# Performance work log

Measured on AMD Instinct MI355X. Metric: run time of the kernel, lower is better.

Reference implementation:

```python
import jax, jax.numpy as jnp
import numpy as np

B, IN_DIM, H, OUT_DIM, T = 2048, 1024, 2048, 1024, 10


def setup_inputs() -> dict:
    key = jax.random.key(0)
    ks = jax.random.split(key, 16)
    s = lambda d: 1.0 / np.sqrt(d)
    inp = {
        "x": jax.random.normal(ks[0], (B, IN_DIM), jnp.float32),
        "z0": jax.random.normal(ks[1], (B, H), jnp.float32),
        "noise": jax.random.normal(ks[2], (T, B, H), jnp.float32),
        # input_embed: Linear(IN,H) -> SiLU -> Linear(H,H)
        "w1_in": jax.random.normal(ks[3], (IN_DIM, H), jnp.float32) * s(IN_DIM),
        "b1_in": jnp.zeros((H,), jnp.float32),
        "w2_in": jax.random.normal(ks[4], (H, H), jnp.float32) * s(H),
        "b2_in": jnp.zeros((H,), jnp.float32),
        # T blocks: Linear(2H,H) -> SiLU -> Linear(H,H), stacked over T
        "wA": jax.random.normal(ks[5], (T, 2 * H, H), jnp.float32) * s(2 * H),
        "bA": jnp.zeros((T, H), jnp.float32),
        "wB": jax.random.normal(ks[6], (T, H, H), jnp.float32) * s(H),
        "bB": jnp.zeros((T, H), jnp.float32),
        # classifier Linear(H, OUT)
        "wC": jax.random.normal(ks[7], (H, OUT_DIM), jnp.float32) * s(H),
        "bC": jnp.zeros((OUT_DIM,), jnp.float32),
    }
    return inp


def _forward(x, z0, noise, w1_in, b1_in, w2_in, b2_in, wA, bA, wB, bB, wC, bC):
    # input embedding
    h = jax.nn.silu(x @ w1_in + b1_in)
    x_embed = h @ w2_in + b2_in  # (B, H)

    alpha = jnp.linspace(0.99, 0.9, T).astype(x.dtype)          # (T,)
    noise_scale = jnp.sqrt(1.0 - alpha)                          # (T,)

    def step(z, per_t):
        wA_t, bA_t, wB_t, bB_t, n_t, a_t, ns_t = per_t
        u = jax.nn.silu(jnp.concatenate([z, x_embed], axis=-1) @ wA_t + bA_t)
        u = u @ wB_t + bB_t
        z_next = a_t * u + (1.0 - a_t) * z + ns_t * n_t
        return z_next, None

    z_final, _ = jax.lax.scan(step, z0, (wA, bA, wB, bB, noise, alpha, noise_scale))
    return z_final @ wC + bC  # (B, OUT_DIM)


def reference(x, z0, noise, w1_in, b1_in, w2_in, b2_in, wA, bA, wB, bB, wC, bC):
    return _forward(x, z0, noise, w1_in, b1_in, w2_in, b2_in, wA, bA, wB, bB, wC, bC)
```

## Files before the change

### kernel.cpp

```cpp
#include <hip/hip_runtime.h>
#include <math.h>

typedef _Float16 f16;
typedef _Float16 f16x4 __attribute__((ext_vector_type(4)));
typedef _Float16 f16x8 __attribute__((ext_vector_type(8)));
typedef float f32x4 __attribute__((ext_vector_type(4)));
typedef float fvec4 __attribute__((ext_vector_type(4)));

#define EP_SILU 0
#define EP_LIN  1
#define EP_ZUP  2
#define EP_OUT  3
#define EP_ADDP 4

struct TDesc {
  const float* W;
  f16* WT;
  long long sW, sWT;
  int R, C, nMat;
};

__device__ __forceinline__ void gll16(const void* g, void* l) {
  __builtin_amdgcn_global_load_lds((__attribute__((address_space(1))) void*)g,
                                   (__attribute__((address_space(3))) void*)l,
                                   16, 0, 0);
}

__device__ __forceinline__ void stage_tile(const f16* __restrict__ g, int ld,
                                           f16* ldsTile, int tid, int wid) {
#pragma unroll
  for (int p = 0; p < 2; ++p) {
    int row = p * 64 + (tid >> 2);
    int col = (tid & 3) * 8;
    gll16(g + (size_t)row * ld + col, ldsTile + p * 2048 + wid * 512);
  }
}

__device__ __forceinline__ void stage8(const f16* __restrict__ g, int ld,
                                       f16* ldsTile, int tid) {
  int row = tid >> 2, col = (tid & 3) * 8;
  gll16(g + (size_t)row * ld + col, ldsTile + tid * 8);
}

__device__ __forceinline__ void tpose_tile(const float* __restrict__ W,
                                           f16* __restrict__ WT, int R, int C,
                                           int r0, int c0, f16 (*t)[72],
                                           int tid) {
#pragma unroll
  for (int p = 0; p < 2; ++p) {
    int lin = p * 2048 + tid * 4;
    int r = lin >> 6, c4 = lin & 63;
    fvec4 v = *(const fvec4*)(W + (size_t)(r0 + r) * C + c0 + c4);
    t[c4 + 0][r] = (f16)v[0];
    t[c4 + 1][r] = (f16)v[1];
    t[c4 + 2][r] = (f16)v[2];
    t[c4 + 3][r] = (f16)v[3];
  }
  __syncthreads();
#pragma unroll
  for (int p = 0; p < 2; ++p) {
    int lin = p * 2048 + tid * 4;
    int c = lin >> 6, r4 = lin & 63;
    f16x4 h;
    h[0] = t[c][r4 + 0];
    h[1] = t[c][r4 + 1];
    h[2] = t[c][r4 + 2];
    h[3] = t[c][r4 + 3];
    *(f16x4*)(WT + (size_t)(c0 + c) * R + r0 + r4) = h;
  }
  __syncthreads();
}

__device__ void run_role(const TDesc d, int rid, int nr, f16 (*t)[72],
                         int tid) {
  if (d.nMat <= 0 || d.W == nullptr) return;
  int tR = d.R >> 6, tC = d.C >> 6;
  int tpm = tR * tC, tot = tpm * d.nMat;
  for (int i = rid; i < tot; i += nr) {
    int m = i / tpm, rem = i - m * tpm;
    int r0 = (rem % tR) << 6, c0 = (rem / tR) << 6;
    tpose_tile(d.W + (size_t)m * d.sW, d.WT + (size_t)m * d.sWT, d.R, d.C, r0,
               c0, t, tid);
  }
}

#define GEMM8_ITER(KP, VM, DO_STAGE)                                          \
  {                                                                           \
    asm volatile("s_waitcnt vmcnt(" #VM ")" ::: "memory");                    \
    __builtin_amdgcn_s_barrier();                                             \
    const int slot_ = (KP) & 1;                                               \
    const f16* LA_ = base + slot_ * 16384 + h * 4096;                         \
    const f16* LB_ = base + slot_ * 16384 + 8192 + h * 4096;                  \
    f16x8 a_[4], b_[4];                                                       \
    _Pragma("unroll") for (int m_ = 0; m_ < 4; ++m_) a_[m_] =                 \
        *(const f16x8*)(LA_ + ((wr * 64 + m_ * 16 + lr) * 32 + kg * 8));      \
    _Pragma("unroll") for (int n_ = 0; n_ < 4; ++n_) b_[n_] =                 \
        *(const f16x8*)(LB_ + ((wc * 64 + n_ * 16 + lr) * 32 + kg * 8));      \
    asm volatile("s_waitcnt lgkmcnt(0)" ::: "memory");                        \
    __builtin_amdgcn_s_barrier();                                             \
    if (DO_STAGE) stageAB((KP) + 2, slot_);                                   \
    _Pragma("unroll") for (int m_ = 0; m_ < 4; ++m_)                          \
        _Pragma("unroll") for (int n_ = 0; n_ < 4; ++n_) acc[m_][n_] =        \
            __builtin_amdgcn_mfma_f32_16x16x32_f16(a_[m_], b_[n_],            \
                                                   acc[m_][n_], 0, 0, 0);     \
  }

template <int EP>
__global__ void __launch_bounds__(512)
gemm8(const f16* __restrict__ A, int lda, const f16* __restrict__ BT, int ldb,
      long long sBT, int K, int N, int gx, int nbGemm,
      const float* __restrict__ bias, long long sBias,
      const f16* __restrict__ addP, f16* __restrict__ outH,
      float* __restrict__ outF, long long sOut, const f16* __restrict__ zOld,
      const float* __restrict__ noise, float aT, float nsT, TDesc dA,
      TDesc dB) {
  __shared__ __align__(16) char smem[65536];
  const int tid = threadIdx.x;
  const int bid = blockIdx.x;

  if (bid >= nbGemm) {
    if (blockIdx.z == 0) {
      int rid = bid - nbGemm, nr = (int)gridDim.x - nbGemm;
      f16(*t)[72] = reinterpret_cast<f16(*)[72]>(smem);
      run_role(dA, rid, nr, t, tid);
      run_role(dB, rid, nr, t, tid);
    }
    return;
  }

  const int z = blockIdx.z;
  const f16* BTz = BT + (size_t)z * sBT;
  f16* outHz = outH ? outH + (size_t)z * sOut : nullptr;
  float* outFz = outF ? outF + (size_t)z * sOut : nullptr;

  const int cpx = nbGemm >> 3;
  const int swz = (bid & 7) * cpx + (bid >> 3);
  const int by = swz / gx, bx = swz % gx;
  const int m0 = by * 128, n0 = bx * 128;

  const int lane = tid & 63, wid = tid >> 6;
  const int q = wid & 3, h = wid >> 2;
  const int wr = q >> 1, wc = q & 1;
  const int lr = lane & 15, kg = lane >> 4;

  f16* base = (f16*)smem;
  f32x4 acc[4][4] = {};

  const int nkp = K >> 6;
  auto stageAB = [&](int kp, int slot) {
    int k0 = kp << 6;
    f16* s = base + slot * 16384;
    stage8(A + (size_t)m0 * lda + k0, lda, s, tid);
    stage8(A + (size_t)m0 * lda + k0 + 32, lda, s + 4096, tid);
    stage8(BTz + (size_t)n0 * ldb + k0, ldb, s + 8192, tid);
    stage8(BTz + (size_t)n0 * ldb + k0 + 32, ldb, s + 12288, tid);
  };

  stageAB(0, 0);
  stageAB(1, 1);
  int kp = 0;
  for (; kp < nkp - 1; ++kp) GEMM8_ITER(kp, 4, (kp + 2 < nkp));
  GEMM8_ITER(kp, 0, 0);

  float* red = (float*)smem;
  if (h == 1) {
#pragma unroll
    for (int m = 0; m < 4; ++m)
#pragma unroll
      for (int n = 0; n < 4; ++n) {
        int row = wr * 64 + m * 16 + kg * 4;
        int col = wc * 64 + n * 16 + lr;
        int rs = row ^ ((col & 7) << 2);
        *(f32x4*)&red[(size_t)col * 128 + rs] = acc[m][n];
      }
  }
  __syncthreads();
  if (h != 0) return;

  float bcol[4];
  if constexpr (EP != EP_ADDP) {
    const float* biasz = bias + (size_t)z * sBias;
#pragma unroll
    for (int n = 0; n < 4; ++n) bcol[n] = biasz[n0 + wc * 64 + n * 16 + lr];
  }

#pragma unroll
  for (int m = 0; m < 4; ++m) {
    int rowb = m0 + wr * 64 + m * 16 + kg * 4;
    int rowl = wr * 64 + m * 16 + kg * 4;
#pragma unroll
    for (int n = 0; n < 4; ++n) {
      int col = n0 + wc * 64 + n * 16 + lr;
      int coll = wc * 64 + n * 16 + lr;
      int rsl = rowl ^ ((coll & 7) << 2);
      f32x4 osum = acc[m][n] + *(const f32x4*)&red[(size_t)coll * 128 + rsl];
#pragma unroll
      for (int r = 0; r < 4; ++r) {
        size_t idx = (size_t)(rowb + r) * N + col;
        float v = osum[r];
        if constexpr (EP == EP_ADDP) v += (float)addP[idx];
        else v += bcol[n];
        if constexpr (EP == EP_SILU || EP == EP_ADDP) {
          v = v / (1.0f + __expf(-v));
          outHz[idx] = (f16)v;
        } else if constexpr (EP == EP_LIN) {
          outHz[idx] = (f16)v;
        } else if constexpr (EP == EP_OUT) {
          outFz[idx] = v;
        } else {
          float zn = aT * v + (1.0f - aT) * (float)zOld[idx] + nsT * noise[idx];
          outHz[idx] = (f16)zn;
        }
      }
    }
  }
}

template <int EP>
__global__ void __launch_bounds__(256)
gemm_bt(const f16* __restrict__ A0, const f16* __restrict__ A1, int Ksplit,
        int lda, const f16* __restrict__ BT, int ldb, long long sBT, int K,
        int N, int gx, const float* __restrict__ bias, long long sBias,
        f16* __restrict__ outH, float* __restrict__ outF, long long sOut,
        const float* __restrict__ zOld, const float* __restrict__ noise,
        float aT, float nsT) {
  __shared__ __align__(16) f16 lds[2][2][128 * 32];
  const int tid = threadIdx.x;
  const int z = blockIdx.z;
  const f16* BTz = BT + (size_t)z * sBT;
  f16* outHz = outH ? outH + (size_t)z * sOut : nullptr;
  float* outFz = outF ? outF + (size_t)z * sOut : nullptr;

  const int lane = tid & 63, wid = tid >> 6;
  const int wr = wid >> 1, wc = wid & 1;
  const int lr = lane & 15, kg = lane >> 4;
  const int by = blockIdx.x / gx, bx = blockIdx.x - by * gx;
  const int m0 = by * 128, n0 = bx * 128;

  f32x4 acc[4][4] = {};
  const int nk = K >> 5;
  auto stageAB = [&](int kt, int buf) {
    int k0 = kt << 5;
    const f16* Abase = (k0 < Ksplit)
                           ? (A0 + (size_t)m0 * lda + k0)
                           : (A1 + (size_t)m0 * lda + (k0 - Ksplit));
    stage_tile(Abase, lda, &lds[buf][0][0], tid, wid);
    stage_tile(BTz + (size_t)n0 * ldb + k0, ldb, &lds[buf][1][0], tid, wid);
  };

  stageAB(0, 0);
  __syncthreads();
  int cur = 0;
  for (int kt = 0; kt < nk; ++kt) {
    if (kt + 1 < nk) stageAB(kt + 1, cur ^ 1);
    const f16* LA = &lds[cur][0][0];
    const f16* LB = &lds[cur][1][0];
    f16x8 a[4], b[4];
#pragma unroll
    for (int m = 0; m < 4; ++m)
      a[m] = *(const f16x8*)(LA + ((wr * 64 + m * 16 + lr) * 32 + kg * 8));
#pragma unroll
    for (int n = 0; n < 4; ++n)
      b[n] = *(const f16x8*)(LB + ((wc * 64 + n * 16 + lr) * 32 + kg * 8));
#pragma unroll
    for (int m = 0; m < 4; ++m)
#pragma unroll
      for (int n = 0; n < 4; ++n)
        acc[m][n] = __builtin_amdgcn_mfma_f32_16x16x32_f16(a[m], b[n],
                                                           acc[m][n], 0, 0, 0);
    __syncthreads();
    cur ^= 1;
  }

  float bcol[4];
  const float* biasz = bias + (size_t)z * sBias;
#pragma unroll
  for (int n = 0; n < 4; ++n) bcol[n] = biasz[n0 + wc * 64 + n * 16 + lr];

#pragma unroll
  for (int m = 0; m < 4; ++m) {
    int rowb = m0 + wr * 64 + m * 16 + kg * 4;
#pragma unroll
    for (int n = 0; n < 4; ++n) {
      int col = n0 + wc * 64 + n * 16 + lr;
#pragma unroll
      for (int r = 0; r < 4; ++r) {
        size_t idx = (size_t)(rowb + r) * N + col;
        float v = acc[m][n][r] + bcol[n];
        if constexpr (EP == EP_SILU) {
          v = v / (1.0f + __expf(-v));
          outHz[idx] = (f16)v;
        } else if constexpr (EP == EP_LIN) {
          outHz[idx] = (f16)v;
        } else if constexpr (EP == EP_OUT) {
          outFz[idx] = v;
        } else {
          float zn = aT * v + (1.0f - aT) * zOld[idx] + nsT * noise[idx];
          outFz[idx] = zn;
          outHz[idx] = (f16)zn;
        }
      }
    }
  }
}

__global__ void __launch_bounds__(512) tconv_role(TDesc d) {
  __shared__ __align__(16) f16 t[64][72];
  run_role(d, blockIdx.x, gridDim.x, t, threadIdx.x);
}

__global__ void __launch_bounds__(256)
cvt4(const float* __restrict__ in, f16* __restrict__ outp, int n4) {
  int i = blockIdx.x * 256 + threadIdx.x;
  if (i >= n4) return;
  fvec4 v = *(const fvec4*)(in + (size_t)i * 4);
  f16x4 h;
  h[0] = (f16)v[0];
  h[1] = (f16)v[1];
  h[2] = (f16)v[2];
  h[3] = (f16)v[3];
  *(f16x4*)(outp + (size_t)i * 4) = h;
}

__global__ void __launch_bounds__(256)
zinit4(const float* __restrict__ z0, float* __restrict__ z32,
       f16* __restrict__ z16, int n4) {
  int i = blockIdx.x * 256 + threadIdx.x;
  if (i >= n4) return;
  fvec4 v = *(const fvec4*)(z0 + (size_t)i * 4);
  *(fvec4*)(z32 + (size_t)i * 4) = v;
  f16x4 h;
  h[0] = (f16)v[0];
  h[1] = (f16)v[1];
  h[2] = (f16)v[2];
  h[3] = (f16)v[3];
  *(f16x4*)(z16 + (size_t)i * 4) = h;
}

extern "C" void kernel_launch(void* const* d_in, const int* in_sizes, int n_in,
                              void* d_out, int out_size, void* d_ws,
                              size_t ws_size, hipStream_t stream) {
  const int B = 2048, IN = 1024, H = 2048, OUT = 1024, T = 10;
  const float* x = (const float*)d_in[0];
  const float* z0 = (const float*)d_in[1];
  const float* noise = (const float*)d_in[2];
  const float* w1 = (const float*)d_in[3];
  const float* b1 = (const float*)d_in[4];
  const float* w2 = (const float*)d_in[5];
  const float* b2 = (const float*)d_in[6];
  const float* wA = (const float*)d_in[7];
  const float* bA = (const float*)d_in[8];
  const float* wB = (const float*)d_in[9];
  const float* bB = (const float*)d_in[10];
  const float* wC = (const float*)d_in[11];
  const float* bC = (const float*)d_in[12];
  float* out = (float*)d_out;

  char* ws = (char*)d_ws;
  size_t off = 0;
  auto alloc = [&](size_t bytes) {
    void* p = ws + off;
    off += (bytes + 255) & ~(size_t)255;
    return p;
  };
  TDesc none = {nullptr, nullptr, 0, 0, 0, 0, 0};

  const size_t FAST_NEED = 273000000ull;
  if (ws_size >= FAST_NEED) {
    f16* x16 = (f16*)alloc((size_t)B * IN * 2);
    f16* h16 = (f16*)alloc((size_t)B * H * 2);
    f16* xe16 = (f16*)alloc((size_t)B * H * 2);
    f16* z16 = (f16*)alloc((size_t)B * H * 2);
    f16* u16 = (f16*)alloc((size_t)B * H * 2);
    f16* p16 = (f16*)alloc((size_t)T * B * H * 2);
    f16* w1T = (f16*)alloc((size_t)IN * H * 2);
    f16* w2T = (f16*)alloc((size_t)H * H * 2);
    f16* wCT = (f16*)alloc((size_t)H * OUT * 2);
    f16* wAbotT = (f16*)alloc((size_t)T * H * H * 2);
    f16* wAtopT[2] = {(f16*)alloc((size_t)H * H * 2),
                      (f16*)alloc((size_t)H * H * 2)};
    f16* wBT2[2] = {(f16*)alloc((size_t)H * H * 2),
                    (f16*)alloc((size_t)H * H * 2)};

    cvt4<<<B * IN / 4 / 256, 256, 0, stream>>>(x, x16, B * IN / 4);
    cvt4<<<B * H / 4 / 256, 256, 0, stream>>>(z0, z16, B * H / 4);
    tconv_role<<<512, 512, 0, stream>>>(TDesc{w1, w1T, 0, 0, IN, H, 1});

    gemm8<EP_SILU><<<512, 512, 0, stream>>>(
        x16, IN, w1T, IN, 0, IN, H, 16, 256, b1, 0, nullptr, h16, nullptr, 0,
        nullptr, nullptr, 0.f, 0.f, TDesc{w2, w2T, 0, 0, H, H, 1},
        TDesc{wA + (size_t)H * H, wAbotT, (long long)2 * H * H,
              (long long)H * H, H, H, 4});
    gemm8<EP_LIN><<<512, 512, 0, stream>>>(
        h16, H, w2T, H, 0, H, H, 16, 256, b2, 0, nullptr, xe16, nullptr, 0,
        nullptr, nullptr, 0.f, 0.f, TDesc{wC, wCT, 0, 0, H, OUT, 1},
        TDesc{wA + (size_t)H * H + (size_t)4 * 2 * H * H,
              wAbotT + (size_t)4 * H * H, (long long)2 * H * H,
              (long long)H * H, H, H, 6});
    tconv_role<<<512, 512, 0, stream>>>(TDesc{wA, wAtopT[0], 0, 0, H, H, 1});

    gemm8<EP_LIN><<<dim3(256, 1, T), 512, 0, stream>>>(
        xe16, H, wAbotT, H, (long long)H * H, H, H, 16, 256, bA, H, nullptr,
        p16, nullptr, (long long)B * H, nullptr, nullptr, 0.f, 0.f, none,
        none);

    for (int t = 0; t < T; ++t) {
      float alpha = (float)(0.99 - 0.01 * (double)t);
      float ns = sqrtf(1.0f - alpha);
      gemm8<EP_ADDP><<<320, 512, 0, stream>>>(
          z16, H, wAtopT[t & 1], H, 0, H, H, 16, 256, nullptr, 0,
          p16 + (size_t)t * B * H, u16, nullptr, 0, nullptr, nullptr, 0.f,
          0.f, TDesc{wB + (size_t)t * H * H, wBT2[t & 1], 0, 0, H, H, 1},
          none);
      TDesc nextA = (t < T - 1)
                        ? TDesc{wA + (size_t)(t + 1) * 2 * H * H,
                                wAtopT[(t + 1) & 1], 0, 0, H, H, 1}
                        : none;
      gemm8<EP_ZUP><<<320, 512, 0, stream>>>(
          u16, H, wBT2[t & 1], H, 0, H, H, 16, 256, bB + (size_t)t * H, 0,
          nullptr, z16, nullptr, 0, z16, noise + (size_t)t * B * H, alpha, ns,
          nextA, none);
    }
    gemm8<EP_OUT><<<128, 512, 0, stream>>>(
        z16, H, wCT, H, 0, H, OUT, 8, 128, bC, 0, nullptr, nullptr, out, 0,
        nullptr, nullptr, 0.f, 0.f, none, none);
  } else {
    f16* x16 = (f16*)alloc((size_t)B * IN * 2);
    f16* h16 = (f16*)alloc((size_t)B * H * 2);
    f16* xe16 = (f16*)alloc((size_t)B * H * 2);
    f16* z16 = (f16*)alloc((size_t)B * H * 2);
    f16* u16 = (f16*)alloc((size_t)B * H * 2);
    float* z32 = (float*)alloc((size_t)B * H * 4);
    f16* w1T = (f16*)alloc((size_t)IN * H * 2);
    f16* w2T = (f16*)alloc((size_t)H * H * 2);
    f16* wCT = (f16*)alloc((size_t)H * OUT * 2);
    f16* wAT = (f16*)alloc((size_t)2 * H * H * 2);
    f16* wBT = (f16*)alloc((size_t)H * H * 2);

    cvt4<<<B * IN / 4 / 256, 256, 0, stream>>>(x, x16, B * IN / 4);
    zinit4<<<B * H / 4 / 256, 256, 0, stream>>>(z0, z32, z16, B * H / 4);
    tconv_role<<<512, 512, 0, stream>>>(TDesc{w1, w1T, 0, 0, IN, H, 1});
    tconv_role<<<1024, 512, 0, stream>>>(TDesc{w2, w2T, 0, 0, H, H, 1});
    tconv_role<<<512, 512, 0, stream>>>(TDesc{wC, wCT, 0, 0, H, OUT, 1});

    gemm_bt<EP_SILU><<<dim3(256, 1, 1), 256, 0, stream>>>(
        x16, x16, IN, IN, w1T, IN, 0, IN, H, 16, b1, 0, h16, nullptr, 0,
        nullptr, nullptr, 0.f, 0.f);
    gemm_bt<EP_LIN><<<dim3(256, 1, 1), 256, 0, stream>>>(
        h16, h16, H, H, w2T, H, 0, H, H, 16, b2, 0, xe16, nullptr, 0, nullptr,
        nullptr, 0.f, 0.f);

    for (int t = 0; t < T; ++t) {
      float alpha = (float)(0.99 - 0.01 * (double)t);
      float ns = sqrtf(1.0f - alpha);
      tconv_role<<<1024, 512, 0, stream>>>(
          TDesc{wA + (size_t)t * 2 * H * H, wAT, 0, 0, 2 * H, H, 1});
      gemm_bt<EP_SILU><<<dim3(256, 1, 1), 256, 0, stream>>>(
          z16, xe16, H, H, wAT, 2 * H, 0, 2 * H, H, 16, bA + (size_t)t * H, 0,
          u16, nullptr, 0, nullptr, nullptr, 0.f, 0.f);
      tconv_role<<<1024, 512, 0, stream>>>(
          TDesc{wB + (size_t)t * H * H, wBT, 0, 0, H, H, 1});
      gemm_bt<EP_ZUP><<<dim3(256, 1, 1), 256, 0, stream>>>(
          u16, u16, H, H, wBT, H, 0, H, H, 16, bB + (size_t)t * H, 0, z16,
          z32, 0, z32, noise + (size_t)t * B * H, alpha, ns);
    }
    gemm_bt<EP_OUT><<<dim3(128, 1, 1), 256, 0, stream>>>(
        z16, z16, H, H, wCT, H, 0, H, OUT, 8, bC, 0, nullptr, out, 0, nullptr,
        nullptr, 0.f, 0.f);
  }
}
```

Before: 1.148 ms.

## Replace split-K 512-thread GEMM with 64x128-tile 256-thread GEMM and swizzled LDS

Replaces the 8-wave, 128x128-tile GEMM, which split K across two wave halves and reduced them through LDS, with a 4-wave kernel using 64x128 tiles, K-step 32, double buffering and XOR-swizzled LDS addressing. Grid sizes double so more blocks cover the 256 CUs, the cross-wave reduction is gone, and the transpose helper kernels move to 256 threads. In exchange, each block reuses fewer A rows per staged B tile, the loop synchronises once per shorter K step, and the explicit vmcnt-based prefetch pipelining is dropped.

```diff
diff --git a/kernel.cpp b/kernel.cpp
--- a/kernel.cpp
+++ b/kernel.cpp
@@ -36,19 +36,13 @@
   }
 }
 
-__device__ __forceinline__ void stage8(const f16* __restrict__ g, int ld,
-                                       f16* ldsTile, int tid) {
-  int row = tid >> 2, col = (tid & 3) * 8;
-  gll16(g + (size_t)row * ld + col, ldsTile + tid * 8);
-}
-
 __device__ __forceinline__ void tpose_tile(const float* __restrict__ W,
                                            f16* __restrict__ WT, int R, int C,
                                            int r0, int c0, f16 (*t)[72],
                                            int tid) {
 #pragma unroll
-  for (int p = 0; p < 2; ++p) {
-    int lin = p * 2048 + tid * 4;
+  for (int p = 0; p < 4; ++p) {
+    int lin = p * 1024 + tid * 4;
     int r = lin >> 6, c4 = lin & 63;
     fvec4 v = *(const fvec4*)(W + (size_t)(r0 + r) * C + c0 + c4);
     t[c4 + 0][r] = (f16)v[0];
@@ -58,8 +52,8 @@
   }
   __syncthreads();
 #pragma unroll
-  for (int p = 0; p < 2; ++p) {
-    int lin = p * 2048 + tid * 4;
+  for (int p = 0; p < 4; ++p) {
+    int lin = p * 1024 + tid * 4;
     int c = lin >> 6, r4 = lin & 63;
     f16x4 h;
     h[0] = t[c][r4 + 0];
@@ -84,37 +78,16 @@
   }
 }
 
-#define GEMM8_ITER(KP, VM, DO_STAGE)                                          \
-  {                                                                           \
-    asm volatile("s_waitcnt vmcnt(" #VM ")" ::: "memory");                    \
-    __builtin_amdgcn_s_barrier();                                             \
-    const int slot_ = (KP) & 1;                                               \
-    const f16* LA_ = base + slot_ * 16384 + h * 4096;                         \
-    const f16* LB_ = base + slot_ * 16384 + 8192 + h * 4096;                  \
-    f16x8 a_[4], b_[4];                                                       \
-    _Pragma("unroll") for (int m_ = 0; m_ < 4; ++m_) a_[m_] =                 \
-        *(const f16x8*)(LA_ + ((wr * 64 + m_ * 16 + lr) * 32 + kg * 8));      \
-    _Pragma("unroll") for (int n_ = 0; n_ < 4; ++n_) b_[n_] =                 \
-        *(const f16x8*)(LB_ + ((wc * 64 + n_ * 16 + lr) * 32 + kg * 8));      \
-    asm volatile("s_waitcnt lgkmcnt(0)" ::: "memory");                        \
-    __builtin_amdgcn_s_barrier();                                             \
-    if (DO_STAGE) stageAB((KP) + 2, slot_);                                   \
-    _Pragma("unroll") for (int m_ = 0; m_ < 4; ++m_)                          \
-        _Pragma("unroll") for (int n_ = 0; n_ < 4; ++n_) acc[m_][n_] =        \
-            __builtin_amdgcn_mfma_f32_16x16x32_f16(a_[m_], b_[n_],            \
-                                                   acc[m_][n_], 0, 0, 0);     \
-  }
-
 template <int EP>
-__global__ void __launch_bounds__(512)
-gemm8(const f16* __restrict__ A, int lda, const f16* __restrict__ BT, int ldb,
+__global__ void __launch_bounds__(256)
+gemm4(const f16* __restrict__ A, int lda, const f16* __restrict__ BT, int ldb,
       long long sBT, int K, int N, int gx, int nbGemm,
       const float* __restrict__ bias, long long sBias,
       const f16* __restrict__ addP, f16* __restrict__ outH,
       float* __restrict__ outF, long long sOut, const f16* __restrict__ zOld,
       const float* __restrict__ noise, float aT, float nsT, TDesc dA,
       TDesc dB) {
-  __shared__ __align__(16) char smem[65536];
+  __shared__ __align__(16) char smem[24576];
   const int tid = threadIdx.x;
   const int bid = blockIdx.x;
 
@@ -136,46 +109,62 @@
   const int cpx = nbGemm >> 3;
   const int swz = (bid & 7) * cpx + (bid >> 3);
   const int by = swz / gx, bx = swz % gx;
-  const int m0 = by * 128, n0 = bx * 128;
+  const int m0 = by * 64, n0 = bx * 128;
 
   const int lane = tid & 63, wid = tid >> 6;
-  const int q = wid & 3, h = wid >> 2;
-  const int wr = q >> 1, wc = q & 1;
+  const int wr = wid >> 1, wc = wid & 1;
   const int lr = lane & 15, kg = lane >> 4;
-
-  f16* base = (f16*)smem;
-  f32x4 acc[4][4] = {};
-
-  const int nkp = K >> 6;
-  auto stageAB = [&](int kp, int slot) {
-    int k0 = kp << 6;
-    f16* s = base + slot * 16384;
-    stage8(A + (size_t)m0 * lda + k0, lda, s, tid);
-    stage8(A + (size_t)m0 * lda + k0 + 32, lda, s + 4096, tid);
-    stage8(BTz + (size_t)n0 * ldb + k0, ldb, s + 8192, tid);
-    stage8(BTz + (size_t)n0 * ldb + k0 + 32, ldb, s + 12288, tid);
+  const int xq = (lr >> 1) & 3;
+
+  f16* lds = (f16*)smem;
+  f32x4 acc[2][4] = {};
+
+  const int nk = K >> 5;
+  auto stageAB = [&](int kt, int buf) {
+    int k0 = kt << 5;
+    f16* sA = lds + buf * 6144;
+    f16* sB = sA + 2048;
+    {
+      int row = tid >> 2;
+      int q = (tid & 3) ^ ((tid >> 3) & 3);
+      gll16(A + (size_t)(m0 + row) * lda + k0 + q * 8, sA + tid * 8);
+    }
+#pragma unroll
+    for (int p = 0; p < 2; ++p) {
+      int pos = p * 256 + tid;
+      int row = pos >> 2;
+      int q = (pos & 3) ^ ((pos >> 3) & 3);
+      gll16(BTz + (size_t)(n0 + row) * ldb + k0 + q * 8, sB + pos * 8);
+    }
   };
 
   stageAB(0, 0);
-  stageAB(1, 1);
-  int kp = 0;
-  for (; kp < nkp - 1; ++kp) GEMM8_ITER(kp, 4, (kp + 2 < nkp));
-  GEMM8_ITER(kp, 0, 0);
-
-  float* red = (float*)smem;
-  if (h == 1) {
-#pragma unroll
-    for (int m = 0; m < 4; ++m)
-#pragma unroll
-      for (int n = 0; n < 4; ++n) {
-        int row = wr * 64 + m * 16 + kg * 4;
-        int col = wc * 64 + n * 16 + lr;
-        int rs = row ^ ((col & 7) << 2);
-        *(f32x4*)&red[(size_t)col * 128 + rs] = acc[m][n];
-      }
-  }
   __syncthreads();
-  if (h != 0) return;
+  int cur = 0;
+  for (int kt = 0; kt < nk; ++kt) {
+    if (kt + 1 < nk) stageAB(kt + 1, cur ^ 1);
+    const f16* LA = lds + cur * 6144;
+    const f16* LB = LA + 2048;
+    f16x8 a[2], b[4];
+#pragma unroll
+    for (int m = 0; m < 2; ++m) {
+      int row = wr * 32 + m * 16 + lr;
+      a[m] = *(const f16x8*)(LA + row * 32 + (kg ^ xq) * 8);
+    }
+#pragma unroll
+    for (int n = 0; n < 4; ++n) {
+      int row = wc * 64 + n * 16 + lr;
+      b[n] = *(const f16x8*)(LB + row * 32 + (kg ^ xq) * 8);
+    }
+#pragma unroll
+    for (int m = 0; m < 2; ++m)
+#pragma unroll
+      for (int n = 0; n < 4; ++n)
+        acc[m][n] = __builtin_amdgcn_mfma_f32_16x16x32_f16(a[m], b[n],
+                                                           acc[m][n], 0, 0, 0);
+    __syncthreads();
+    cur ^= 1;
+  }
 
   float bcol[4];
   if constexpr (EP != EP_ADDP) {
@@ -185,19 +174,15 @@
   }
 
 #pragma unroll
-  for (int m = 0; m < 4; ++m) {
-    int rowb = m0 + wr * 64 + m * 16 + kg * 4;
-    int rowl = wr * 64 + m * 16 + kg * 4;
+  for (int m = 0; m < 2; ++m) {
+    int rowb = m0 + wr * 32 + m * 16 + kg * 4;
 #pragma unroll
     for (int n = 0; n < 4; ++n) {
       int col = n0 + wc * 64 + n * 16 + lr;
-      int coll = wc * 64 + n * 16 + lr;
-      int rsl = rowl ^ ((coll & 7) << 2);
-      f32x4 osum = acc[m][n] + *(const f32x4*)&red[(size_t)coll * 128 + rsl];
 #pragma unroll
       for (int r = 0; r < 4; ++r) {
         size_t idx = (size_t)(rowb + r) * N + col;
-        float v = osum[r];
+        float v = acc[m][n][r];
         if constexpr (EP == EP_ADDP) v += (float)addP[idx];
         else v += bcol[n];
         if constexpr (EP == EP_SILU || EP == EP_ADDP) {
@@ -304,7 +289,7 @@
   }
 }
 
-__global__ void __launch_bounds__(512) tconv_role(TDesc d) {
+__global__ void __launch_bounds__(256) tconv_role(TDesc d) {
   __shared__ __align__(16) f16 t[64][72];
   run_role(d, blockIdx.x, gridDim.x, t, threadIdx.x);
 }
@@ -384,31 +369,31 @@
 
     cvt4<<<B * IN / 4 / 256, 256, 0, stream>>>(x, x16, B * IN / 4);
     cvt4<<<B * H / 4 / 256, 256, 0, stream>>>(z0, z16, B * H / 4);
-    tconv_role<<<512, 512, 0, stream>>>(TDesc{w1, w1T, 0, 0, IN, H, 1});
-
-    gemm8<EP_SILU><<<512, 512, 0, stream>>>(
-        x16, IN, w1T, IN, 0, IN, H, 16, 256, b1, 0, nullptr, h16, nullptr, 0,
+    tconv_role<<<512, 256, 0, stream>>>(TDesc{w1, w1T, 0, 0, IN, H, 1});
+
+    gemm4<EP_SILU><<<640, 256, 0, stream>>>(
+        x16, IN, w1T, IN, 0, IN, H, 16, 512, b1, 0, nullptr, h16, nullptr, 0,
         nullptr, nullptr, 0.f, 0.f, TDesc{w2, w2T, 0, 0, H, H, 1},
         TDesc{wA + (size_t)H * H, wAbotT, (long long)2 * H * H,
               (long long)H * H, H, H, 4});
-    gemm8<EP_LIN><<<512, 512, 0, stream>>>(
-        h16, H, w2T, H, 0, H, H, 16, 256, b2, 0, nullptr, xe16, nullptr, 0,
+    gemm4<EP_LIN><<<640, 256, 0, stream>>>(
+        h16, H, w2T, H, 0, H, H, 16, 512, b2, 0, nullptr, xe16, nullptr, 0,
         nullptr, nullptr, 0.f, 0.f, TDesc{wC, wCT, 0, 0, H, OUT, 1},
         TDesc{wA + (size_t)H * H + (size_t)4 * 2 * H * H,
               wAbotT + (size_t)4 * H * H, (long long)2 * H * H,
               (long long)H * H, H, H, 6});
-    tconv_role<<<512, 512, 0, stream>>>(TDesc{wA, wAtopT[0], 0, 0, H, H, 1});
-
-    gemm8<EP_LIN><<<dim3(256, 1, T), 512, 0, stream>>>(
-        xe16, H, wAbotT, H, (long long)H * H, H, H, 16, 256, bA, H, nullptr,
+    tconv_role<<<256, 256, 0, stream>>>(TDesc{wA, wAtopT[0], 0, 0, H, H, 1});
+
+    gemm4<EP_LIN><<<dim3(512, 1, T), 256, 0, stream>>>(
+        xe16, H, wAbotT, H, (long long)H * H, H, H, 16, 512, bA, H, nullptr,
         p16, nullptr, (long long)B * H, nullptr, nullptr, 0.f, 0.f, none,
         none);
 
     for (int t = 0; t < T; ++t) {
       float alpha = (float)(0.99 - 0.01 * (double)t);
       float ns = sqrtf(1.0f - alpha);
-      gemm8<EP_ADDP><<<320, 512, 0, stream>>>(
-          z16, H, wAtopT[t & 1], H, 0, H, H, 16, 256, nullptr, 0,
+      gemm4<EP_ADDP><<<576, 256, 0, stream>>>(
+          z16, H, wAtopT[t & 1], H, 0, H, H, 16, 512, nullptr, 0,
           p16 + (size_t)t * B * H, u16, nullptr, 0, nullptr, nullptr, 0.f,
           0.f, TDesc{wB + (size_t)t * H * H, wBT2[t & 1], 0, 0, H, H, 1},
           none);
@@ -416,13 +401,13 @@
                         ? TDesc{wA + (size_t)(t + 1) * 2 * H * H,
                                 wAtopT[(t + 1) & 1], 0, 0, H, H, 1}
                         : none;
-      gemm8<EP_ZUP><<<320, 512, 0, stream>>>(
-          u16, H, wBT2[t & 1], H, 0, H, H, 16, 256, bB + (size_t)t * H, 0,
+      gemm4<EP_ZUP><<<576, 256, 0, stream>>>(
+          u16, H, wBT2[t & 1], H, 0, H, H, 16, 512, bB + (size_t)t * H, 0,
           nullptr, z16, nullptr, 0, z16, noise + (size_t)t * B * H, alpha, ns,
           nextA, none);
     }
-    gemm8<EP_OUT><<<128, 512, 0, stream>>>(
-        z16, H, wCT, H, 0, H, OUT, 8, 128, bC, 0, nullptr, nullptr, out, 0,
+    gemm4<EP_OUT><<<256, 256, 0, stream>>>(
+        z16, H, wCT, H, 0, H, OUT, 8, 256, bC, 0, nullptr, nullptr, out, 0,
         nullptr, nullptr, 0.f, 0.f, none, none);
   } else {
     f16* x16 = (f16*)alloc((size_t)B * IN * 2);
@@ -439,9 +424,9 @@
 
     cvt4<<<B * IN / 4 / 256, 256, 0, stream>>>(x, x16, B * IN / 4);
     zinit4<<<B * H / 4 / 256, 256, 0, stream>>>(z0, z32, z16, B * H / 4);
-    tconv_role<<<512, 512, 0, stream>>>(TDesc{w1, w1T, 0, 0, IN, H, 1});
-    tconv_role<<<1024, 512, 0, stream>>>(TDesc{w2, w2T, 0, 0, H, H, 1});
-    tconv_role<<<512, 512, 0, stream>>>(TDesc{wC, wCT, 0, 0, H, OUT, 1});
+    tconv_role<<<512, 256, 0, stream>>>(TDesc{w1, w1T, 0, 0, IN, H, 1});
+    tconv_role<<<1024, 256, 0, stream>>>(TDesc{w2, w2T, 0, 0, H, H, 1});
+    tconv_role<<<512, 256, 0, stream>>>(TDesc{wC, wCT, 0, 0, H, OUT, 1});
 
     gemm_bt<EP_SILU><<<dim3(256, 1, 1), 256, 0, stream>>>(
         x16, x16, IN, IN, w1T, IN, 0, IN, H, 16, b1, 0, h16, nullptr, 0,
@@ -453,12 +438,12 @@
     for (int t = 0; t < T; ++t) {
       float alpha = (float)(0.99 - 0.01 * (double)t);
       float ns = sqrtf(1.0f - alpha);
-      tconv_role<<<1024, 512, 0, stream>>>(
+      tconv_role<<<1024, 256, 0, stream>>>(
           TDesc{wA + (size_t)t * 2 * H * H, wAT, 0, 0, 2 * H, H, 1});
       gemm_bt<EP_SILU><<<dim3(256, 1, 1), 256, 0, stream>>>(
           z16, xe16, H, H, wAT, 2 * H, 0, 2 * H, H, 16, bA + (size_t)t * H, 0,
           u16, nullptr, 0, nullptr, nullptr, 0.f, 0.f);
-      tconv_role<<<1024, 512, 0, stream>>>(
+      tconv_role<<<1024, 256, 0, stream>>>(
           TDesc{wB + (size_t)t * H * H, wBT, 0, 0, H, H, 1});
       gemm_bt<EP_ZUP><<<dim3(256, 1, 1), 256, 0, stream>>>(
           u16, u16, H, H, wBT, H, 0, H, H, 16, bB + (size_t)t * H, 0, z16,
```

Result: slower. 1.316 ms (+14.6%).
